# Kernel optimization log

Measured on AMD Instinct MI355X. Metric: run time of the kernel, lower is better.

Reference implementation:

```python
import jax, jax.numpy as jnp
import numpy as np

WINDOW_SIZE = 8
NUM_HEADS = 6
SHIFT_SIZE = 0


def rel_pos_log(ws):
    # torch.meshgrid default is 'ij' indexing
    coords = jnp.stack(jnp.meshgrid(jnp.arange(ws), jnp.arange(ws), indexing='ij'))  # [2,ws,ws]
    flat = coords.reshape(2, -1)                      # [2, N]
    rel = flat[:, :, None] - flat[:, None, :]          # [2, N, N]
    rel = rel.transpose(1, 2, 0).astype(jnp.float32)   # [N, N, 2]
    return jnp.sign(rel) * jnp.log1p(jnp.abs(rel))


def setup_inputs() -> dict:
    key = jax.random.key(0)
    k0, k1, k2, k3 = jax.random.split(key, 4)
    B_, N, dim, H = 2048, WINDOW_SIZE * WINDOW_SIZE, 192, NUM_HEADS
    qkv = jax.random.normal(k0, (B_, N, 3 * dim), dtype=jnp.float32)
    qkv_mfif = jax.random.normal(k1, (B_, N, 3 * dim), dtype=jnp.float32)
    W1 = jax.random.normal(k2, (2, 256), dtype=jnp.float32) * 0.1
    b1 = jnp.zeros((256,), dtype=jnp.float32)
    W2 = jax.random.normal(k3, (256, H), dtype=jnp.float32) * 0.1
    b2 = jnp.zeros((H,), dtype=jnp.float32)
    return {"qkv": qkv, "qkv_mfif": qkv_mfif, "W1": W1, "b1": b1,
            "W2": W2, "b2": b2, "trainingTag": 2}


def _split_heads(t, H):
    B_, N, C3 = t.shape
    dim = C3 // 3
    hd = dim // H
    t = t.reshape(B_, N, 3, H, hd).transpose(2, 0, 3, 1, 4)  # [3, B_, H, N, hd]
    return t[0], t[1], t[2]


def _forward(qkv, qkv_mfif, W1, b1, W2, b2, trainingTag):
    sg = jax.lax.stop_gradient
    H = NUM_HEADS
    B_, N, C3 = qkv.shape
    dim = C3 // 3
    hd = dim // H
    scale = hd ** (-0.5)

    q, k, v = _split_heads(qkv, H)
    qm, km, vm = _split_heads(qkv_mfif, H)

    # relative position bias from tiny MLP: [N,N,2] -> [N,N,H] -> [H,N,N]
    rp = rel_pos_log(WINDOW_SIZE)
    bias = jax.nn.relu(rp @ W1 + b1) @ W2 + b2
    bias = bias.transpose(2, 0, 1)[None]  # [1,H,N,N]

    if trainingTag == 2:
        q = sg(q * scale)
        qm = qm * scale
        if SHIFT_SIZE == 0:
            attn = sg(jnp.einsum('bhnd,bhmd->bhnm', qm, k))
        else:
            attn = sg(jnp.einsum('bhnd,bhmd->bhnm', q, k))
        attn_m = jnp.einsum('bhnd,bhmd->bhnm', qm, km)
        attn = sg(jax.nn.softmax(attn + sg(bias), axis=-1))
        attn_m = jax.nn.softmax(attn_m + bias, axis=-1)
        x_ivif = sg(jnp.einsum('bhnm,bhmd->bhnd', attn, v).transpose(0, 2, 1, 3).reshape(B_, N, dim))
        x_mfif = jnp.einsum('bhnm,bhmd->bhnd', attn_m, vm).transpose(0, 2, 1, 3).reshape(B_, N, dim)
    else:  # trainingTag == 1
        q = q * scale
        qm = sg(qm * scale)
        attn = jnp.einsum('bhnd,bhmd->bhnm', q, k)
        if SHIFT_SIZE == 0:
            attn_m = sg(jnp.einsum('bhnd,bhmd->bhnm', q, km))
        else:
            attn_m = sg(jnp.einsum('bhnd,bhmd->bhnm', qm, km))
        attn = jax.nn.softmax(attn + bias, axis=-1)
        attn_m = sg(jax.nn.softmax(attn_m + bias, axis=-1))
        x_ivif = jnp.einsum('bhnm,bhmd->bhnd', attn, v).transpose(0, 2, 1, 3).reshape(B_, N, dim)
        x_mfif = sg(jnp.einsum('bhnm,bhmd->bhnd', attn_m, vm).transpose(0, 2, 1, 3).reshape(B_, N, dim))
    return x_ivif, x_mfif


def reference(qkv, qkv_mfif, W1, b1, W2, b2, trainingTag):
    return _forward(qkv, qkv_mfif, W1, b1, W2, b2, trainingTag)
```

## Files before the change

### kernel.cpp

```cpp
#include <hip/hip_runtime.h>


typedef float  f32x4  __attribute__((ext_vector_type(4)));
typedef short  bf16x8 __attribute__((ext_vector_type(8)));
typedef unsigned short u16x8 __attribute__((ext_vector_type(8)));
typedef unsigned short u16x4 __attribute__((ext_vector_type(4)));

__device__ __forceinline__ unsigned short f2bf(float f) {
  unsigned int u = __builtin_bit_cast(unsigned int, f);
  unsigned int r = (u + 0x7FFFu + ((u >> 16) & 1u)) >> 16;
  return (unsigned short)r;
}

__global__ void bias_mlp_kernel(const float* __restrict__ W1,
                                const float* __restrict__ b1,
                                const float* __restrict__ W2,
                                const float* __restrict__ b2,
                                float* __restrict__ bias_ws) {
  int idx  = blockIdx.x * 256 + threadIdx.x;
  int reg  = idx & 3;
  int lane = (idx >> 2) & 63;
  int tile = (idx >> 8) & 15;
  int h    = idx >> 12;
  int mt = tile >> 2, nt = tile & 3;
  int n = nt * 16 + (lane & 15);
  int m = mt * 16 + (lane >> 4) * 4 + reg;
  float dr = (float)((n >> 3) - (m >> 3));
  float dc = (float)((n & 7) - (m & 7));
  float fr = copysignf(log1pf(fabsf(dr)), dr);
  float fc = copysignf(log1pf(fabsf(dc)), dc);
  float acc = b2[h];
  for (int jj = 0; jj < 256; ++jj) {
    float hid = fmaf(fr, W1[jj], fmaf(fc, W1[256 + jj], b1[jj]));
    hid = fmaxf(hid, 0.0f);
    acc = fmaf(hid, W2[jj * 6 + h], acc);
  }
  bias_ws[idx] = acc;
}

__global__ __launch_bounds__(256, 6)
void wattn_kernel(const float* __restrict__ qkv,
                  const float* __restrict__ mfif,
                  const float* __restrict__ bias_ws,
                  const int*   __restrict__ tagp,
                  float* __restrict__ out) {
  const int bid  = blockIdx.x;
  const int h    = bid % 6;
  const int b    = bid / 6;
  const int tid  = threadIdx.x;
  const int lane = tid & 63;
  const int w    = tid >> 6;
  const int j    = lane & 15;
  const int g    = lane >> 4;

  __shared__ unsigned short k_s [64][36];
  __shared__ unsigned short km_s[64][36];
  __shared__ unsigned short vT_s[2][32][66];
  __shared__ unsigned short P_s [64][66];
  __shared__ __align__(16) float sums_s[2][64];

  const int tag = *tagp;
  const float* qsrc = (tag == 2) ? mfif : qkv;
  const size_t base = (size_t)b * 36864;
  const float scale = 0.17677669529663687f;

  const int n_k = tid >> 2, seg = tid & 3;
  const int d_v = tid & 31, m0_v = (tid >> 5) * 8;

  const float* pq = qsrc + base + (size_t)(16 * w + j) * 576 + h * 32 + g * 8;
  f32x4 qA = *(const f32x4*)pq;
  f32x4 qB = *(const f32x4*)(pq + 4);

  const float* pk = qkv + base + (size_t)n_k * 576 + 192 + h * 32 + seg * 8;
  f32x4 kA = *(const f32x4*)pk;
  f32x4 kB = *(const f32x4*)(pk + 4);

  const float* pm = mfif + base + (size_t)n_k * 576 + 192 + h * 32 + seg * 8;
  f32x4 mA = *(const f32x4*)pm;
  f32x4 mB = *(const f32x4*)(pm + 4);

  const float* pv  = qkv  + base + 384 + h * 32 + d_v;
  const float* pvm = mfif + base + 384 + h * 32 + d_v;
  float vv[8], vmv[8];
#pragma unroll
  for (int e = 0; e < 8; ++e) vv[e]  = pv [(size_t)(m0_v + e) * 576];
#pragma unroll
  for (int e = 0; e < 8; ++e) vmv[e] = pvm[(size_t)(m0_v + e) * 576];

  f32x4 bias4[4];
#pragma unroll
  for (int mt = 0; mt < 4; ++mt)
    bias4[mt] = *(const f32x4*)&bias_ws[(((h * 16) + mt * 4 + w) * 64 + lane) * 4];

  __builtin_amdgcn_sched_barrier(0);

  bf16x8 bq;
  {
    u16x8 oq;
#pragma unroll
    for (int e = 0; e < 4; ++e) {
      oq[e]     = f2bf(qA[e] * scale);
      oq[e + 4] = f2bf(qB[e] * scale);
    }
    bq = __builtin_bit_cast(bf16x8, oq);
  }
  {
    u16x8 ok, om;
#pragma unroll
    for (int e = 0; e < 4; ++e) {
      ok[e] = f2bf(kA[e]);  ok[e + 4] = f2bf(kB[e]);
      om[e] = f2bf(mA[e]);  om[e + 4] = f2bf(mB[e]);
    }
    *(u16x8*)&k_s [n_k][seg * 8] = ok;
    *(u16x8*)&km_s[n_k][seg * 8] = om;
  }
  {
    u16x8 ov, om;
#pragma unroll
    for (int e = 0; e < 8; ++e) { ov[e] = f2bf(vv[e]); om[e] = f2bf(vmv[e]); }
    *(u16x8*)&vT_s[0][d_v][m0_v] = ov;
    *(u16x8*)&vT_s[1][d_v][m0_v] = om;
  }
  __syncthreads();

#pragma unroll
  for (int s = 0; s < 2; ++s) {
    const unsigned short (*Ks)[36] = (s == 0) ? k_s : km_s;

    f32x4 acc[4];
#pragma unroll
    for (int mt = 0; mt < 4; ++mt) {
      bf16x8 ak = *(const bf16x8*)&Ks[mt * 16 + j][g * 8];
      acc[mt] = __builtin_amdgcn_mfma_f32_16x16x32_bf16(ak, bq, bias4[mt], 0, 0, 0);
    }

    float t0 = 0.f, t1 = 0.f, t2 = 0.f, t3 = 0.f;
#pragma unroll
    for (int mt = 0; mt < 4; ++mt) {
      float e0 = __expf(acc[mt][0]);
      float e1 = __expf(acc[mt][1]);
      float e2 = __expf(acc[mt][2]);
      float e3 = __expf(acc[mt][3]);
      u16x4 pw;
      pw[0] = f2bf(e0); pw[1] = f2bf(e1); pw[2] = f2bf(e2); pw[3] = f2bf(e3);
      *(u16x4*)&P_s[16 * w + j][mt * 16 + g * 4] = pw;
      t0 += e0; t1 += e1; t2 += e2; t3 += e3;
    }
    float sum = (t0 + t1) + (t2 + t3);
    sum += __shfl_xor(sum, 16);
    sum += __shfl_xor(sum, 32);
    if (g == 0) sums_s[s][16 * w + j] = sum;

    f32x4 xo[2] = {{0.f, 0.f, 0.f, 0.f}, {0.f, 0.f, 0.f, 0.f}};
#pragma unroll
    for (int kt = 0; kt < 2; ++kt) {
      bf16x8 ap = *(const bf16x8*)&P_s[16 * w + j][kt * 32 + g * 8];
#pragma unroll
      for (int dt = 0; dt < 2; ++dt) {
        bf16x8 bv = *(const bf16x8*)&vT_s[s][16 * dt + j][kt * 32 + g * 8];
        xo[dt] = __builtin_amdgcn_mfma_f32_16x16x32_bf16(ap, bv, xo[dt], 0, 0, 0);
      }
    }

    f32x4 sm = *(const f32x4*)&sums_s[s][16 * w + 4 * g];
    float inv[4];
#pragma unroll
    for (int r = 0; r < 4; ++r) inv[r] = __builtin_amdgcn_rcpf(sm[r]);
    float* ob = out + (size_t)s * 25165824 + (size_t)b * 12288 + h * 32;
#pragma unroll
    for (int dt = 0; dt < 2; ++dt)
#pragma unroll
      for (int r = 0; r < 4; ++r)
        ob[(16 * w + g * 4 + r) * 192 + dt * 16 + j] = xo[dt][r] * inv[r];
  }
}

extern "C" void kernel_launch(void* const* d_in, const int* in_sizes, int n_in,
                              void* d_out, int out_size, void* d_ws, size_t ws_size,
                              hipStream_t stream) {
  const float* qkv  = (const float*)d_in[0];
  const float* mfif = (const float*)d_in[1];
  const float* W1   = (const float*)d_in[2];
  const float* b1   = (const float*)d_in[3];
  const float* W2   = (const float*)d_in[4];
  const float* b2   = (const float*)d_in[5];
  const int*   tag  = (const int*)d_in[6];
  float* out     = (float*)d_out;
  float* bias_ws = (float*)d_ws;

  hipLaunchKernelGGL(bias_mlp_kernel, dim3(96), dim3(256), 0, stream,
                     W1, b1, W2, b2, bias_ws);
  hipLaunchKernelGGL(wattn_kernel, dim3(12288), dim3(256), 0, stream,
                     qkv, mfif, bias_ws, tag, out);
}
```

Before: 156.6 us.

## Stage K/V tiles via direct global-to-LDS loads with XOR swizzle

K, Km, V and Vm tiles are now copied straight from global memory into LDS as fp32 using global_load_lds, with an XOR-swizzled layout. The bf16 conversion moves to the point where each wave reads operands for the MFMAs. This removes the register round trip and the separate transpose store for V. In exchange LDS use roughly doubles, which is why launch bounds drop to 3 blocks per CU. Each wave also repeats the conversion work and does scalar strided LDS reads for V.

```diff
diff --git a/kernel.cpp b/kernel.cpp
--- a/kernel.cpp
+++ b/kernel.cpp
@@ -11,6 +11,11 @@
   unsigned int r = (u + 0x7FFFu + ((u >> 16) & 1u)) >> 16;
   return (unsigned short)r;
 }
+
+#define GLD16(gp, lp)                                                         \
+  __builtin_amdgcn_global_load_lds(                                           \
+      (const __attribute__((address_space(1))) unsigned int*)(gp),            \
+      (__attribute__((address_space(3))) unsigned int*)(lp), 16, 0, 0)
 
 __global__ void bias_mlp_kernel(const float* __restrict__ W1,
                                 const float* __restrict__ b1,
@@ -38,7 +43,7 @@
   bias_ws[idx] = acc;
 }
 
-__global__ __launch_bounds__(256, 6)
+__global__ __launch_bounds__(256, 3)
 void wattn_kernel(const float* __restrict__ qkv,
                   const float* __restrict__ mfif,
                   const float* __restrict__ bias_ws,
@@ -53,10 +58,11 @@
   const int j    = lane & 15;
   const int g    = lane >> 4;
 
-  __shared__ unsigned short k_s [64][36];
-  __shared__ unsigned short km_s[64][36];
-  __shared__ unsigned short vT_s[2][32][66];
-  __shared__ unsigned short P_s [64][66];
+  __shared__ float k_f [64][32];
+  __shared__ float km_f[64][32];
+  __shared__ float v_f [64][32];
+  __shared__ float vm_f[64][32];
+  __shared__ unsigned short P_s[64][66];
   __shared__ __align__(16) float sums_s[2][64];
 
   const int tag = *tagp;
@@ -64,38 +70,27 @@
   const size_t base = (size_t)b * 36864;
   const float scale = 0.17677669529663687f;
 
-  const int n_k = tid >> 2, seg = tid & 3;
-  const int d_v = tid & 31, m0_v = (tid >> 5) * 8;
-
-  const float* pq = qsrc + base + (size_t)(16 * w + j) * 576 + h * 32 + g * 8;
-  f32x4 qA = *(const f32x4*)pq;
-  f32x4 qB = *(const f32x4*)(pq + 4);
-
-  const float* pk = qkv + base + (size_t)n_k * 576 + 192 + h * 32 + seg * 8;
-  f32x4 kA = *(const f32x4*)pk;
-  f32x4 kB = *(const f32x4*)(pk + 4);
-
-  const float* pm = mfif + base + (size_t)n_k * 576 + 192 + h * 32 + seg * 8;
-  f32x4 mA = *(const f32x4*)pm;
-  f32x4 mB = *(const f32x4*)(pm + 4);
-
-  const float* pv  = qkv  + base + 384 + h * 32 + d_v;
-  const float* pvm = mfif + base + 384 + h * 32 + d_v;
-  float vv[8], vmv[8];
+  {
+    const int ldsb = ((tid >> 6) * 64) * 16;
 #pragma unroll
-  for (int e = 0; e < 8; ++e) vv[e]  = pv [(size_t)(m0_v + e) * 576];
-#pragma unroll
-  for (int e = 0; e < 8; ++e) vmv[e] = pvm[(size_t)(m0_v + e) * 576];
-
-  f32x4 bias4[4];
-#pragma unroll
-  for (int mt = 0; mt < 4; ++mt)
-    bias4[mt] = *(const f32x4*)&bias_ws[(((h * 16) + mt * 4 + w) * 64 + lane) * 4];
-
-  __builtin_amdgcn_sched_barrier(0);
+    for (int it = 0; it < 2; ++it) {
+      const int c   = it * 256 + tid;
+      const int row = c >> 3;
+      const int sl  = c & 7;
+      const size_t gof = base + (size_t)row * 576 + ((sl ^ (row & 7)) * 4) + h * 32;
+      const int lb = it * 4096 + ldsb;
+      GLD16(qkv  + gof + 192, (char*)&k_f [0][0] + lb);
+      GLD16(mfif + gof + 192, (char*)&km_f[0][0] + lb);
+      GLD16(qkv  + gof + 384, (char*)&v_f [0][0] + lb);
+      GLD16(mfif + gof + 384, (char*)&vm_f[0][0] + lb);
+    }
+  }
 
   bf16x8 bq;
   {
+    const float* pq = qsrc + base + (size_t)(16 * w + j) * 576 + h * 32 + g * 8;
+    f32x4 qA = *(const f32x4*)pq;
+    f32x4 qB = *(const f32x4*)(pq + 4);
     u16x8 oq;
 #pragma unroll
     for (int e = 0; e < 4; ++e) {
@@ -104,34 +99,30 @@
     }
     bq = __builtin_bit_cast(bf16x8, oq);
   }
-  {
-    u16x8 ok, om;
+  f32x4 bias4[4];
 #pragma unroll
-    for (int e = 0; e < 4; ++e) {
-      ok[e] = f2bf(kA[e]);  ok[e + 4] = f2bf(kB[e]);
-      om[e] = f2bf(mA[e]);  om[e + 4] = f2bf(mB[e]);
-    }
-    *(u16x8*)&k_s [n_k][seg * 8] = ok;
-    *(u16x8*)&km_s[n_k][seg * 8] = om;
-  }
-  {
-    u16x8 ov, om;
-#pragma unroll
-    for (int e = 0; e < 8; ++e) { ov[e] = f2bf(vv[e]); om[e] = f2bf(vmv[e]); }
-    *(u16x8*)&vT_s[0][d_v][m0_v] = ov;
-    *(u16x8*)&vT_s[1][d_v][m0_v] = om;
-  }
+  for (int mt = 0; mt < 4; ++mt)
+    bias4[mt] = *(const f32x4*)&bias_ws[(((h * 16) + mt * 4 + w) * 64 + lane) * 4];
+
   __syncthreads();
 
 #pragma unroll
   for (int s = 0; s < 2; ++s) {
-    const unsigned short (*Ks)[36] = (s == 0) ? k_s : km_s;
+    const float (*Kf)[32] = s ? km_f : k_f;
+    const float (*Vf)[32] = s ? vm_f : v_f;
 
     f32x4 acc[4];
 #pragma unroll
     for (int mt = 0; mt < 4; ++mt) {
-      bf16x8 ak = *(const bf16x8*)&Ks[mt * 16 + j][g * 8];
-      acc[mt] = __builtin_amdgcn_mfma_f32_16x16x32_bf16(ak, bq, bias4[mt], 0, 0, 0);
+      const int row = mt * 16 + j;
+      const int x   = j & 7;
+      f32x4 a0 = *(const f32x4*)&Kf[row][((2 * g) ^ x) * 4];
+      f32x4 a1 = *(const f32x4*)&Kf[row][((2 * g + 1) ^ x) * 4];
+      u16x8 ok;
+#pragma unroll
+      for (int e = 0; e < 4; ++e) { ok[e] = f2bf(a0[e]); ok[e + 4] = f2bf(a1[e]); }
+      acc[mt] = __builtin_amdgcn_mfma_f32_16x16x32_bf16(
+          __builtin_bit_cast(bf16x8, ok), bq, bias4[mt], 0, 0, 0);
     }
 
     float t0 = 0.f, t1 = 0.f, t2 = 0.f, t3 = 0.f;
@@ -157,8 +148,16 @@
       bf16x8 ap = *(const bf16x8*)&P_s[16 * w + j][kt * 32 + g * 8];
 #pragma unroll
       for (int dt = 0; dt < 2; ++dt) {
-        bf16x8 bv = *(const bf16x8*)&vT_s[s][16 * dt + j][kt * 32 + g * 8];
-        xo[dt] = __builtin_amdgcn_mfma_f32_16x16x32_bf16(ap, bv, xo[dt], 0, 0, 0);
+        const int col = dt * 16 + j;
+        const int cq  = col >> 2, cr = col & 3;
+        u16x8 ov;
+#pragma unroll
+        for (int e = 0; e < 8; ++e) {
+          const int row = kt * 32 + g * 8 + e;
+          ov[e] = f2bf(Vf[row][((cq ^ e) * 4) + cr]);
+        }
+        xo[dt] = __builtin_amdgcn_mfma_f32_16x16x32_bf16(
+            ap, __builtin_bit_cast(bf16x8, ov), xo[dt], 0, 0, 0);
       }
     }
 
```

After: 152.8 us. -2.4%, faster.
